# Optimization experiments

Hardware: AMD Instinct MI355X
Metric: run time of the kernel (lower is better)

## Reference

```python
import jax, jax.numpy as jnp
import numpy as np

N = 100000
E = 1600000
FEAT, COND, HID, LAT = 128, 32, 128, 64


def _init(key, shape, fan_in):
    # glorot-ish init, scale irrelevant for correctness baseline
    return jax.random.normal(key, shape, dtype=jnp.float32) / np.sqrt(fan_in)


def setup_inputs() -> dict:
    key = jax.random.key(0)
    ks = jax.random.split(key, 20)
    inp = {
        "feature": jax.random.normal(ks[0], (N, FEAT), dtype=jnp.float32),
        "condition": jax.random.normal(ks[1], (N, COND), dtype=jnp.float32),
        "noise": jax.random.normal(ks[2], (N, LAT), dtype=jnp.float32),
        "edge_index": jax.random.randint(ks[3], (2, E), 0, N, dtype=jnp.int64),
        # encoder GCNConv params (PyG convention: out = (norm-agg of x @ W) + b)
        "enc_i2h_W": _init(ks[4], (FEAT + COND, HID), FEAT + COND),
        "enc_i2h_b": jnp.zeros((HID,), jnp.float32),
        "enc_h2h_W": _init(ks[5], (HID, HID), HID),
        "enc_h2h_b": jnp.zeros((HID,), jnp.float32),
        "enc_mean_W": _init(ks[6], (HID, LAT), HID),
        "enc_mean_b": jnp.zeros((LAT,), jnp.float32),
        "enc_logvar_W": _init(ks[7], (HID, LAT), HID),
        "enc_logvar_b": jnp.zeros((LAT,), jnp.float32),
        # decoder GCNConv params
        "dec_i2h_W": _init(ks[8], (LAT + COND, HID), LAT + COND),
        "dec_i2h_b": jnp.zeros((HID,), jnp.float32),
        "dec_h2h_W": _init(ks[9], (HID, HID), HID),
        "dec_h2h_b": jnp.zeros((HID,), jnp.float32),
        "dec_out_W": _init(ks[10], (HID, FEAT), HID),
        "dec_out_b": jnp.zeros((FEAT,), jnp.float32),
    }
    return inp


def _gcn_prep(edge_index, n):
    # add self loops, compute symmetric normalization D^{-1/2} (A+I) D^{-1/2}
    loop = jnp.arange(n, dtype=edge_index.dtype)
    src = jnp.concatenate([edge_index[0], loop])  # [E+N]
    dst = jnp.concatenate([edge_index[1], loop])
    deg = jax.ops.segment_sum(jnp.ones_like(dst, dtype=jnp.float32), dst, num_segments=n)
    dis = jnp.where(deg > 0, jax.lax.rsqrt(deg), 0.0)
    norm = dis[src] * dis[dst]  # [E+N]
    return src, dst, norm


def _gcn_conv(x, W, b, src, dst, norm, n):
    h = x @ W                           # [N, out]
    msg = h[src] * norm[:, None]        # gather + scale, [E+N, out]
    out = jax.ops.segment_sum(msg, dst, num_segments=n)  # scatter-add
    return out + b


def reference(feature, condition, noise, edge_index,
              enc_i2h_W, enc_i2h_b, enc_h2h_W, enc_h2h_b,
              enc_mean_W, enc_mean_b, enc_logvar_W, enc_logvar_b,
              dec_i2h_W, dec_i2h_b, dec_h2h_W, dec_h2h_b,
              dec_out_W, dec_out_b):
    n = feature.shape[0]
    src, dst, norm = _gcn_prep(edge_index, n)
    # encoder
    x = jnp.concatenate([feature, condition], axis=1)
    h = jnp.tanh(_gcn_conv(x, enc_i2h_W, enc_i2h_b, src, dst, norm, n))
    h = jnp.tanh(_gcn_conv(h, enc_h2h_W, enc_h2h_b, src, dst, norm, n))
    mean = _gcn_conv(h, enc_mean_W, enc_mean_b, src, dst, norm, n)
    logvar = _gcn_conv(h, enc_logvar_W, enc_logvar_b, src, dst, norm, n)
    z = noise * jnp.exp(0.5 * logvar) + mean
    # decoder
    x2 = jnp.concatenate([z, condition], axis=1)
    g = jnp.tanh(_gcn_conv(x2, dec_i2h_W, dec_i2h_b, src, dst, norm, n))
    g = jnp.tanh(_gcn_conv(g, dec_h2h_W, dec_h2h_b, src, dst, norm, n))
    out = _gcn_conv(g, dec_out_W, dec_out_b, src, dst, norm, n)
    return (z, mean, logvar, out)
```

## Files before the change

### kernel.cpp

```cpp
#include <hip/hip_runtime.h>
#include <hip/hip_fp16.h>
#include <math.h>


#define FEAT 128
#define COND 32
#define HID  128
#define LAT  64

#define NG    8
#define RANGE 12500
#define BPG   32

typedef _Float16 f16x8 __attribute__((ext_vector_type(8)));
typedef float f32x4 __attribute__((ext_vector_type(4)));
typedef float floatx2 __attribute__((ext_vector_type(2)));

__device__ __forceinline__ uint pk2(float x, float y) {
  __half2 h = __floats2half2_rn(x, y);
  return __builtin_bit_cast(uint, h);
}
__device__ __forceinline__ floatx2 up8(uint u) {
  return __builtin_amdgcn_cvt_pk_f32_fp8(u, false);
}
__device__ __forceinline__ uint pk8(float a, float b) {
  return (uint)__builtin_amdgcn_cvt_pk_fp8_f32(a, b, 0, false);
}
__device__ __forceinline__ unsigned char pk8b(float a) {
  return (unsigned char)(pk8(a, a) & 0xff);
}

__global__ __launch_bounds__(256) void k_hist(const int* __restrict__ dstArr,
                                              int* __restrict__ part, int E, int n) {
  __shared__ int bins[RANGE];
  const int g = blockIdx.x & (NG - 1), bi = blockIdx.x >> 3;
  const int lo = g * RANGE;
  const int hi = min(n, lo + RANGE);
  for (int ii = threadIdx.x; ii < RANGE; ii += 256) bins[ii] = 0;
  __syncthreads();
  const int quads = E >> 2;
  const int per = (quads + BPG - 1) / BPG;
  const int q0 = bi * per, q1 = min(quads, q0 + per);
  const int4* d4 = (const int4*)dstArr;
  for (int q = q0 + threadIdx.x; q < q1; q += 256) {
    int4 d = d4[q];
    if (d.x >= lo && d.x < hi) atomicAdd(&bins[d.x - lo], 1);
    if (d.y >= lo && d.y < hi) atomicAdd(&bins[d.y - lo], 1);
    if (d.z >= lo && d.z < hi) atomicAdd(&bins[d.z - lo], 1);
    if (d.w >= lo && d.w < hi) atomicAdd(&bins[d.w - lo], 1);
  }
  if (bi == 0) {
    for (int e = (quads << 2) + threadIdx.x; e < E; e += 256) {
      int d = dstArr[e];
      if (d >= lo && d < hi) atomicAdd(&bins[d - lo], 1);
    }
  }
  __syncthreads();
  int* dst = part + (size_t)(g * BPG + bi) * RANGE;
  for (int ii = threadIdx.x; ii < RANGE; ii += 256) dst[ii] = bins[ii];
}

__global__ void k_scan1(const int* __restrict__ part, int* __restrict__ degI,
                        float* __restrict__ dis, int* __restrict__ ptr,
                        int* __restrict__ blkSum, int n) {
  __shared__ int wtot[4];
  int tid = threadIdx.x, lane = tid & 63, wid = tid >> 6;
  int base = blockIdx.x * 1024 + tid * 4;
  int v[4];
#pragma unroll
  for (int j = 0; j < 4; j++) {
    int i = base + j;
    int c = 0;
    if (i < n) {
      int g = i / RANGE, ii = i - g * RANGE;
      const int* p = part + (size_t)g * BPG * RANGE + ii;
      for (int b = 0; b < BPG; b++) c += p[(size_t)b * RANGE];
      degI[i] = c;
      dis[i] = rsqrtf((float)(c + 1));
    }
    v[j] = c;
  }
  int tsum = v[0] + v[1] + v[2] + v[3];
  int x = tsum;
#pragma unroll
  for (int off = 1; off < 64; off <<= 1) {
    int y = __shfl_up(x, off);
    if (lane >= off) x += y;
  }
  if (lane == 63) wtot[wid] = x;
  __syncthreads();
  int wbase = 0;
  for (int w = 0; w < wid; w++) wbase += wtot[w];
  int run = wbase + (x - tsum);
#pragma unroll
  for (int j = 0; j < 4; j++) {
    int i = base + j;
    if (i < n) ptr[i] = run;
    run += v[j];
  }
  if (tid == blockDim.x - 1) blkSum[blockIdx.x] = wbase + x;
}

__global__ void k_scan2(const int* __restrict__ blkSum, int* __restrict__ blkOff, int nb) {
  __shared__ int wtot[4];
  int tid = threadIdx.x, lane = tid & 63, wid = tid >> 6;
  int v = (tid < nb) ? blkSum[tid] : 0;
  int x = v;
#pragma unroll
  for (int off = 1; off < 64; off <<= 1) {
    int y = __shfl_up(x, off);
    if (lane >= off) x += y;
  }
  if (lane == 63) wtot[wid] = x;
  __syncthreads();
  int wbase = 0;
  for (int w = 0; w < wid; w++) wbase += wtot[w];
  if (tid < nb) blkOff[tid] = wbase + x - v;
}

__global__ void k_scan3(int* __restrict__ ptr, const int* __restrict__ blkOff, int n) {
  int i = blockIdx.x * blockDim.x + threadIdx.x;
  if (i < n) ptr[i] += blkOff[i >> 10];
}

__global__ void k_cum(int* __restrict__ part, const int* __restrict__ ptr, int n) {
  int i = blockIdx.x * blockDim.x + threadIdx.x;
  if (i >= n) return;
  int g = i / RANGE, ii = i - g * RANGE;
  int* p = part + (size_t)g * BPG * RANGE + ii;
  int run = ptr[i];
  for (int b = 0; b < BPG; b++) {
    int t = p[(size_t)b * RANGE];
    p[(size_t)b * RANGE] = run;
    run += t;
  }
}

__global__ __launch_bounds__(256) void k_fill2(const int* __restrict__ ei,
                                               const int* __restrict__ part,
                                               int* __restrict__ csr, int E, int n) {
  __shared__ int cur[RANGE];
  const int g = blockIdx.x & (NG - 1), bi = blockIdx.x >> 3;
  const int lo = g * RANGE;
  const int hi = min(n, lo + RANGE);
  const int* base = part + (size_t)(g * BPG + bi) * RANGE;
  for (int ii = threadIdx.x; ii < RANGE; ii += 256) cur[ii] = base[ii];
  __syncthreads();
  const int quads = E >> 2;
  const int per = (quads + BPG - 1) / BPG;
  const int q0 = bi * per, q1 = min(quads, q0 + per);
  const int4* s4 = (const int4*)ei;
  const int4* d4 = (const int4*)(ei + E);
  for (int q = q0 + threadIdx.x; q < q1; q += 256) {
    int4 s = s4[q], d = d4[q];
    if (d.x >= lo && d.x < hi) csr[atomicAdd(&cur[d.x - lo], 1)] = s.x;
    if (d.y >= lo && d.y < hi) csr[atomicAdd(&cur[d.y - lo], 1)] = s.y;
    if (d.z >= lo && d.z < hi) csr[atomicAdd(&cur[d.z - lo], 1)] = s.z;
    if (d.w >= lo && d.w < hi) csr[atomicAdd(&cur[d.w - lo], 1)] = s.w;
  }
  if (bi == 0) {
    for (int e = (quads << 2) + threadIdx.x; e < E; e += 256) {
      int d = ei[E + e];
      if (d >= lo && d < hi) csr[atomicAdd(&cur[d - lo], 1)] = ei[e];
    }
  }
}

__global__ void k_cast8(const float* __restrict__ src, uint* __restrict__ dst,
                        const float* __restrict__ dis, int n4) {
  int t = blockIdx.x * blockDim.x + threadIdx.x;
  if (t >= n4) return;
  size_t i4 = (size_t)t * 4;
  int row = (int)(i4 >> 5);
  float d = dis[row];
  float4 v = *(const float4*)&src[i4];
  uint r = (uint)__builtin_amdgcn_cvt_pk_fp8_f32(d * v.x, d * v.y, 0, false);
  r = (uint)__builtin_amdgcn_cvt_pk_fp8_f32(d * v.z, d * v.w, (int)r, true);
  dst[t] = r;
}

struct PW { const float* src; unsigned short* dst; int K, Ncols, colOff, NnTot; };
struct PWArr { PW d[7]; };

__global__ void k_packw(PWArr a) {
  PW d = a.d[blockIdx.y];
  int t = blockIdx.x * blockDim.x + threadIdx.x;
  if (t >= d.K * d.Ncols) return;
  int k = t / d.Ncols;
  int n = t - k * d.Ncols;
  float v = d.src[t];
  d.dst[((size_t)(k >> 3) * d.NnTot + d.colOff + n) * 8 + (k & 7)] =
      __builtin_bit_cast(unsigned short, (_Float16)v);
}

template <int W, int OUTK>
__global__ __launch_bounds__(256) void k_agg8(
    const unsigned char* __restrict__ X8, void* __restrict__ Yv,
    const int* __restrict__ degI, const float* __restrict__ dis,
    const int* __restrict__ ptr, const int* __restrict__ csr,
    const float* __restrict__ bias, int n) {
  constexpr int LPR = W / 2;
  constexpr int NB = 64 / LPR;
  __shared__ int idxs[4][72];
  const int wvw = threadIdx.x >> 6;
  const int l = threadIdx.x & 63;
  const int sub = l / LPR;
  const int boff = (l % LPR) * 2;
  const unsigned char* __restrict__ Xb = X8 + boff;
  const int stride = gridDim.x * 4;

  for (int i = blockIdx.x * 4 + wvw; i < n; i += stride) {
    const int p0 = ptr[i];
    const int cnt = degI[i];
    if (l < cnt) idxs[wvw][l] = csr[p0 + l];
    floatx2 acc;
    {
      uint u = *(const unsigned short*)(Xb + (size_t)i * W);
      floatx2 f = up8(u);
      acc.x = (sub == 0) ? f.x : 0.f;
      acc.y = (sub == 0) ? f.y : 0.f;
    }
    const int m = min(cnt, 64);
    int e = 0;
    if (NB == 1) {
      for (; e + 8 <= m; e += 8) {
        int4 q0 = *(const int4*)&idxs[wvw][e];
        int4 q1 = *(const int4*)&idxs[wvw][e + 4];
        uint u0 = *(const unsigned short*)(Xb + ((uint)q0.x << 7));
        uint u1 = *(const unsigned short*)(Xb + ((uint)q0.y << 7));
        uint u2 = *(const unsigned short*)(Xb + ((uint)q0.z << 7));
        uint u3 = *(const unsigned short*)(Xb + ((uint)q0.w << 7));
        uint u4 = *(const unsigned short*)(Xb + ((uint)q1.x << 7));
        uint u5 = *(const unsigned short*)(Xb + ((uint)q1.y << 7));
        uint u6 = *(const unsigned short*)(Xb + ((uint)q1.z << 7));
        uint u7 = *(const unsigned short*)(Xb + ((uint)q1.w << 7));
        acc += up8(u0) + up8(u1);
        acc += up8(u2) + up8(u3);
        acc += up8(u4) + up8(u5);
        acc += up8(u6) + up8(u7);
      }
      for (; e < m; ++e) {
        int s = idxs[wvw][e];
        acc += up8(*(const unsigned short*)(Xb + ((uint)s << 7)));
      }
      for (; e < cnt; ++e) {
        int s = csr[p0 + e];
        acc += up8(*(const unsigned short*)(Xb + ((uint)s << 7)));
      }
    } else {
      constexpr int SH = (W == 64) ? 6 : 5;
      for (; e + 4 * NB <= m; e += 4 * NB) {
        int s0 = idxs[wvw][e + sub];
        int s1 = idxs[wvw][e + NB + sub];
        int s2 = idxs[wvw][e + 2 * NB + sub];
        int s3 = idxs[wvw][e + 3 * NB + sub];
        uint u0 = *(const unsigned short*)(Xb + ((uint)s0 << SH));
        uint u1 = *(const unsigned short*)(Xb + ((uint)s1 << SH));
        uint u2 = *(const unsigned short*)(Xb + ((uint)s2 << SH));
        uint u3 = *(const unsigned short*)(Xb + ((uint)s3 << SH));
        acc += up8(u0) + up8(u1);
        acc += up8(u2) + up8(u3);
      }
      for (; e < m; e += NB) {
        int ii = e + sub;
        if (ii < m)
          acc += up8(*(const unsigned short*)(Xb + ((uint)idxs[wvw][ii] << SH)));
      }
      for (; e < cnt; e += NB) {
        int ii = e + sub;
        if (ii < cnt)
          acc += up8(*(const unsigned short*)(Xb + ((uint)csr[p0 + ii] << SH)));
      }
#pragma unroll
      for (int mask = LPR; mask < 64; mask <<= 1) {
        acc.x += __shfl_xor(acc.x, mask);
        acc.y += __shfl_xor(acc.y, mask);
      }
    }
    if (sub == 0) {
      float di = dis[i];
      float a0 = di * acc.x, a1 = di * acc.y;
      if (OUTK == 1) {
        float2 b = *(const float2*)&bias[boff];
        uint p = pk8(di * tanhf(a0 + b.x), di * tanhf(a1 + b.y));
        *(unsigned short*)((unsigned char*)Yv + (size_t)i * W + boff) =
            (unsigned short)p;
      } else {
        *(uint*)((unsigned char*)Yv + ((size_t)i * W + boff) * 2) = pk2(a0, a1);
      }
    }
  }
}

template <int KT, int MODE>
__global__ __launch_bounds__(256) void k_gemm16(
    const _Float16* __restrict__ A1, int K1,
    const _Float16* __restrict__ A2, int K2,
    const unsigned short* __restrict__ Wp,
    const float* __restrict__ b1, const float* __restrict__ b2,
    float* __restrict__ O1, float* __restrict__ O2, float* __restrict__ O3,
    unsigned char* __restrict__ O8,
    const float* __restrict__ noise, const float* __restrict__ dis, int M) {
  __shared__ unsigned short wl[(KT / 8) * 1024];
  const int tid = threadIdx.x;
  const int l = tid & 63, wid = tid >> 6;
  const int row0 = blockIdx.x * 128;
  constexpr int totalU16 = (KT / 8) * 1024;
  for (int o = tid * 8; o < totalU16; o += 256 * 8) {
    *(uint4*)&wl[o] = *(const uint4*)&Wp[o];
  }
  __syncthreads();

  const int ar = l & 15, kg = l >> 4;
  f32x4 acc[2][8] = {};
  for (int k0 = 0; k0 < KT; k0 += 32) {
    const _Float16* Ab;
    int kl, Kb;
    if (k0 < K1) { Ab = A1; kl = k0; Kb = K1; }
    else         { Ab = A2; kl = k0 - K1; Kb = K2; }
    f16x8 a[2];
#pragma unroll
    for (int mt = 0; mt < 2; mt++) {
      int row = row0 + wid * 32 + mt * 16 + ar;
      if (row < M) {
        a[mt] = *(const f16x8*)&Ab[(size_t)row * Kb + kl + kg * 8];
      } else {
#pragma unroll
        for (int j = 0; j < 8; j++) a[mt][j] = (_Float16)0;
      }
    }
    int lb = ((k0 >> 3) + kg) * 1024 + ar * 8;
#pragma unroll
    for (int nt = 0; nt < 8; nt++) {
      f16x8 b = *(const f16x8*)&wl[lb + nt * 128];
#pragma unroll
      for (int mt = 0; mt < 2; mt++)
        acc[mt][nt] = __builtin_amdgcn_mfma_f32_16x16x32_f16(a[mt], b, acc[mt][nt], 0, 0, 0);
    }
  }

#pragma unroll
  for (int mt = 0; mt < 2; mt++) {
    int rbase = row0 + wid * 32 + mt * 16 + (l >> 4) * 4;
#pragma unroll
    for (int r = 0; r < 4; r++) {
      int rw = rbase + r;
      if (rw >= M) continue;
      if (MODE == 1) {
        float dr = dis[rw];
#pragma unroll
        for (int nt = 0; nt < 4; nt++) {
          int c = nt * 16 + (l & 15);
          float mv = acc[mt][nt][r] + b1[c];
          float lv = acc[mt][nt + 4][r] + b2[c];
          O1[(size_t)rw * 64 + c] = mv;
          O2[(size_t)rw * 64 + c] = lv;
          float z = noise[(size_t)rw * 64 + c] * expf(0.5f * lv) + mv;
          O3[(size_t)rw * 64 + c] = z;
          O8[(size_t)rw * 64 + c] = pk8b(dr * z);
        }
      } else if (MODE == 0) {
        float dr = dis[rw];
#pragma unroll
        for (int nt = 0; nt < 8; nt++) {
          int c = nt * 16 + (l & 15);
          float v = tanhf(acc[mt][nt][r] + b1[c]);
          O8[(size_t)rw * 128 + c] = pk8b(dr * v);
        }
      } else {
#pragma unroll
        for (int nt = 0; nt < 8; nt++) {
          int c = nt * 16 + (l & 15);
          O1[(size_t)rw * 128 + c] = acc[mt][nt][r] + b1[c];
        }
      }
    }
  }
}

__global__ __launch_bounds__(256) void k_gemmP1(
    const float* __restrict__ F, const float* __restrict__ Cnd,
    const unsigned short* __restrict__ Wp, unsigned char* __restrict__ O8,
    const float* __restrict__ dis, int M) {
  __shared__ unsigned short wl[20 * 1024];
  const int tid = threadIdx.x;
  const int l = tid & 63, wid = tid >> 6;
  const int row0 = blockIdx.x * 128;
  for (int o = tid * 8; o < 20 * 1024; o += 256 * 8) {
    *(uint4*)&wl[o] = *(const uint4*)&Wp[o];
  }
  __syncthreads();

  const int ar = l & 15, kg = l >> 4;
  f32x4 acc[2][8] = {};
  for (int k0 = 0; k0 < 160; k0 += 32) {
    int col0 = k0 + kg * 8;
    f16x8 a[2];
#pragma unroll
    for (int mt = 0; mt < 2; mt++) {
      int row = row0 + wid * 32 + mt * 16 + ar;
      float4 u = {0, 0, 0, 0}, v = {0, 0, 0, 0};
      if (row < M) {
        if (col0 < 128) {
          u = *(const float4*)&F[(size_t)row * 128 + col0];
          v = *(const float4*)&F[(size_t)row * 128 + col0 + 4];
        } else {
          u = *(const float4*)&Cnd[(size_t)row * 32 + (col0 - 128)];
          v = *(const float4*)&Cnd[(size_t)row * 32 + (col0 - 124)];
        }
      }
      a[mt][0] = (_Float16)u.x; a[mt][1] = (_Float16)u.y;
      a[mt][2] = (_Float16)u.z; a[mt][3] = (_Float16)u.w;
      a[mt][4] = (_Float16)v.x; a[mt][5] = (_Float16)v.y;
      a[mt][6] = (_Float16)v.z; a[mt][7] = (_Float16)v.w;
    }
    int lb = ((k0 >> 3) + kg) * 1024 + ar * 8;
#pragma unroll
    for (int nt = 0; nt < 8; nt++) {
      f16x8 b = *(const f16x8*)&wl[lb + nt * 128];
#pragma unroll
      for (int mt = 0; mt < 2; mt++)
        acc[mt][nt] = __builtin_amdgcn_mfma_f32_16x16x32_f16(a[mt], b, acc[mt][nt], 0, 0, 0);
    }
  }
#pragma unroll
  for (int mt = 0; mt < 2; mt++) {
    int rbase = row0 + wid * 32 + mt * 16 + (l >> 4) * 4;
#pragma unroll
    for (int r = 0; r < 4; r++) {
      int rw = rbase + r;
      if (rw >= M) continue;
      float dr = dis[rw];
#pragma unroll
      for (int nt = 0; nt < 8; nt++) {
        int c = nt * 16 + (l & 15);
        O8[(size_t)rw * 128 + c] = pk8b(dr * acc[mt][nt][r]);
      }
    }
  }
}


static inline size_t align_up(size_t x, size_t a) { return (x + a - 1) & ~(a - 1); }

extern "C" void kernel_launch(void* const* d_in, const int* in_sizes, int n_in,
                              void* d_out, int out_size, void* d_ws, size_t ws_size,
                              hipStream_t stream) {
  const float* feature   = (const float*)d_in[0];
  const float* condition = (const float*)d_in[1];
  const float* noise     = (const float*)d_in[2];
  const int*   ei        = (const int*)d_in[3];
  const float* Wenc1 = (const float*)d_in[4];  const float* benc1 = (const float*)d_in[5];
  const float* Wenc2 = (const float*)d_in[6];  const float* benc2 = (const float*)d_in[7];
  const float* Wm    = (const float*)d_in[8];  const float* bm    = (const float*)d_in[9];
  const float* Wlv   = (const float*)d_in[10]; const float* blv   = (const float*)d_in[11];
  const float* Wd1   = (const float*)d_in[12]; const float* bd1   = (const float*)d_in[13];
  const float* Wd2   = (const float*)d_in[14]; const float* bd2   = (const float*)d_in[15];
  const float* Wout  = (const float*)d_in[16]; const float* bout  = (const float*)d_in[17];

  const int N = in_sizes[0] / FEAT;
  const int E = in_sizes[3] / 2;

  float* out = (float*)d_out;
  float* zseg    = out;
  float* meanseg = out + (size_t)N * LAT;
  float* lvseg   = out + (size_t)2 * N * LAT;
  float* outseg  = out + (size_t)3 * N * LAT;

  char* w = (char*)d_ws;
  size_t off = 0;
  int*   degI   = (int*)(w + off);   off = align_up(off + (size_t)N * 4, 256);
  float* dis    = (float*)(w + off); off = align_up(off + (size_t)N * 4, 256);
  int*   ptr    = (int*)(w + off);   off = align_up(off + (size_t)N * 4, 256);
  int*   blkSum = (int*)(w + off);   off = align_up(off + 4096, 256);
  int*   blkOff = (int*)(w + off);   off = align_up(off + 4096, 256);
  int*   csr    = (int*)(w + off);   off = align_up(off + (size_t)(E + 64) * 4, 256);
  unsigned short* WpE1 = (unsigned short*)(w + off); off = align_up(off + 160 * 128 * 2, 256);
  unsigned short* WpE2 = (unsigned short*)(w + off); off = align_up(off + 128 * 128 * 2, 256);
  unsigned short* WpML = (unsigned short*)(w + off); off = align_up(off + 128 * 128 * 2, 256);
  unsigned short* WpD1 = (unsigned short*)(w + off); off = align_up(off + 96 * 128 * 2, 256);
  unsigned short* WpD2 = (unsigned short*)(w + off); off = align_up(off + 128 * 128 * 2, 256);
  unsigned short* WpO  = (unsigned short*)(w + off); off = align_up(off + 128 * 128 * 2, 256);
  _Float16* S  = (_Float16*)(w + off); off = align_up(off + (size_t)N * 32 * 2, 256);
  _Float16* TA = (_Float16*)(w + off); off = align_up(off + (size_t)N * 128 * 2, 256);
  unsigned char* F8A = (unsigned char*)(w + off); off = align_up(off + (size_t)N * 128, 256);
  unsigned char* F8B = (unsigned char*)(w + off); off = align_up(off + (size_t)N * 128, 256);
  unsigned char* C8  = (unsigned char*)(w + off); off = align_up(off + (size_t)N * 32, 256);
  int* part = (int*)TA;

  const int TB_ = 256;
  dim3 blk(TB_);
  dim3 gN((N + TB_ - 1) / TB_);
  const int nScanBlk = (N + 1023) / 1024;
  dim3 gAgg(2048);
  dim3 gG((N + 127) / 128);
  dim3 gPart(NG * BPG);

  k_hist<<<gPart, blk, 0, stream>>>(ei + E, part, E, N);
  k_scan1<<<dim3(nScanBlk), blk, 0, stream>>>(part, degI, dis, ptr, blkSum, N);
  k_scan2<<<dim3(1), blk, 0, stream>>>(blkSum, blkOff, nScanBlk);
  k_scan3<<<gN, blk, 0, stream>>>(ptr, blkOff, N);
  k_cum<<<gN, blk, 0, stream>>>(part, ptr, N);
  k_fill2<<<gPart, blk, 0, stream>>>(ei, part, csr, E, N);

  k_cast8<<<dim3(((size_t)N * 32 / 4 + TB_ - 1) / TB_), blk, 0, stream>>>(
      condition, (uint*)C8, dis, N * 32 / 4);
  {
    PWArr pa;
    pa.d[0] = {Wenc1, WpE1, 160, 128, 0, 128};
    pa.d[1] = {Wenc2, WpE2, 128, 128, 0, 128};
    pa.d[2] = {Wm,    WpML, 128, 64,  0, 128};
    pa.d[3] = {Wlv,   WpML, 128, 64, 64, 128};
    pa.d[4] = {Wd1,   WpD1,  96, 128, 0, 128};
    pa.d[5] = {Wd2,   WpD2, 128, 128, 0, 128};
    pa.d[6] = {Wout,  WpO,  128, 128, 0, 128};
    k_packw<<<dim3(80, 7), blk, 0, stream>>>(pa);
  }

  k_gemmP1<<<gG, blk, 0, stream>>>(feature, condition, WpE1, F8A, dis, N);
  k_agg8<HID, 1><<<gAgg, blk, 0, stream>>>(F8A, F8B, degI, dis, ptr, csr, benc1, N);
  k_agg8<HID, 0><<<gAgg, blk, 0, stream>>>(F8B, TA, degI, dis, ptr, csr, nullptr, N);
  k_gemm16<128, 0><<<gG, blk, 0, stream>>>(
      TA, HID, nullptr, 0, WpE2, benc2, nullptr,
      nullptr, nullptr, nullptr, F8A, nullptr, dis, N);
  k_agg8<HID, 0><<<gAgg, blk, 0, stream>>>(F8A, TA, degI, dis, ptr, csr, nullptr, N);
  k_gemm16<128, 1><<<gG, blk, 0, stream>>>(
      TA, HID, nullptr, 0, WpML, bm, blv,
      meanseg, lvseg, zseg, F8B, noise, dis, N);

  k_agg8<LAT, 0><<<gAgg, blk, 0, stream>>>(F8B, TA, degI, dis, ptr, csr, nullptr, N);
  k_agg8<COND, 0><<<gAgg, blk, 0, stream>>>(C8, S, degI, dis, ptr, csr, nullptr, N);
  k_gemm16<96, 0><<<gG, blk, 0, stream>>>(
      TA, LAT, S, COND, WpD1, bd1, nullptr,
      nullptr, nullptr, nullptr, F8A, nullptr, dis, N);
  k_agg8<HID, 0><<<gAgg, blk, 0, stream>>>(F8A, TA, degI, dis, ptr, csr, nullptr, N);
  k_gemm16<128, 0><<<gG, blk, 0, stream>>>(
      TA, HID, nullptr, 0, WpD2, bd2, nullptr,
      nullptr, nullptr, nullptr, F8B, nullptr, dis, N);
  k_agg8<HID, 0><<<gAgg, blk, 0, stream>>>(F8B, TA, degI, dis, ptr, csr, nullptr, N);
  k_gemm16<128, 2><<<gG, blk, 0, stream>>>(
      TA, HID, nullptr, 0, WpO, bout, nullptr,
      outseg, nullptr, nullptr, nullptr, nullptr, dis, N);
}
```

Baseline: 614.1 us.

## Reorder decoder first layer to transform-then-aggregate via templated input GEMM

The decoder's first GCN layer used to aggregate z (64 wide) and condition (32 wide) separately, then run the 96-wide GEMM. Now it runs the GEMM on raw z and condition first, producing 128-wide fp8 features, and then aggregates with the fused bias+tanh aggregation used in the encoder. This drops the cast kernel, the condition aggregation and the z fp8 store. The catch is that the aggregation now runs at width 128 instead of 64+32, so there is more gather traffic.

Result: faster. 548.9 us (-10.6%).

```diff
diff --git a/kernel.cpp b/kernel.cpp
--- a/kernel.cpp
+++ b/kernel.cpp
@@ -164,19 +164,6 @@
       if (d >= lo && d < hi) csr[atomicAdd(&cur[d - lo], 1)] = ei[e];
     }
   }
-}
-
-__global__ void k_cast8(const float* __restrict__ src, uint* __restrict__ dst,
-                        const float* __restrict__ dis, int n4) {
-  int t = blockIdx.x * blockDim.x + threadIdx.x;
-  if (t >= n4) return;
-  size_t i4 = (size_t)t * 4;
-  int row = (int)(i4 >> 5);
-  float d = dis[row];
-  float4 v = *(const float4*)&src[i4];
-  uint r = (uint)__builtin_amdgcn_cvt_pk_fp8_f32(d * v.x, d * v.y, 0, false);
-  r = (uint)__builtin_amdgcn_cvt_pk_fp8_f32(d * v.z, d * v.w, (int)r, true);
-  dst[t] = r;
 }
 
 struct PW { const float* src; unsigned short* dst; int K, Ncols, colOff, NnTot; };
@@ -347,7 +334,6 @@
       int rw = rbase + r;
       if (rw >= M) continue;
       if (MODE == 1) {
-        float dr = dis[rw];
 #pragma unroll
         for (int nt = 0; nt < 4; nt++) {
           int c = nt * 16 + (l & 15);
@@ -357,7 +343,6 @@
           O2[(size_t)rw * 64 + c] = lv;
           float z = noise[(size_t)rw * 64 + c] * expf(0.5f * lv) + mv;
           O3[(size_t)rw * 64 + c] = z;
-          O8[(size_t)rw * 64 + c] = pk8b(dr * z);
         }
       } else if (MODE == 0) {
         float dr = dis[rw];
@@ -378,22 +363,25 @@
   }
 }
 
+template <int KT, int KA>
 __global__ __launch_bounds__(256) void k_gemmP1(
-    const float* __restrict__ F, const float* __restrict__ Cnd,
+    const float* __restrict__ A, const float* __restrict__ B,
     const unsigned short* __restrict__ Wp, unsigned char* __restrict__ O8,
     const float* __restrict__ dis, int M) {
-  __shared__ unsigned short wl[20 * 1024];
+  constexpr int KB = KT - KA;
+  __shared__ unsigned short wl[(KT / 8) * 1024];
   const int tid = threadIdx.x;
   const int l = tid & 63, wid = tid >> 6;
   const int row0 = blockIdx.x * 128;
-  for (int o = tid * 8; o < 20 * 1024; o += 256 * 8) {
+  constexpr int totalU16 = (KT / 8) * 1024;
+  for (int o = tid * 8; o < totalU16; o += 256 * 8) {
     *(uint4*)&wl[o] = *(const uint4*)&Wp[o];
   }
   __syncthreads();
 
   const int ar = l & 15, kg = l >> 4;
   f32x4 acc[2][8] = {};
-  for (int k0 = 0; k0 < 160; k0 += 32) {
+  for (int k0 = 0; k0 < KT; k0 += 32) {
     int col0 = k0 + kg * 8;
     f16x8 a[2];
 #pragma unroll
@@ -401,12 +389,12 @@
       int row = row0 + wid * 32 + mt * 16 + ar;
       float4 u = {0, 0, 0, 0}, v = {0, 0, 0, 0};
       if (row < M) {
-        if (col0 < 128) {
-          u = *(const float4*)&F[(size_t)row * 128 + col0];
-          v = *(const float4*)&F[(size_t)row * 128 + col0 + 4];
+        if (col0 < KA) {
+          u = *(const float4*)&A[(size_t)row * KA + col0];
+          v = *(const float4*)&A[(size_t)row * KA + col0 + 4];
         } else {
-          u = *(const float4*)&Cnd[(size_t)row * 32 + (col0 - 128)];
-          v = *(const float4*)&Cnd[(size_t)row * 32 + (col0 - 124)];
+          u = *(const float4*)&B[(size_t)row * KB + (col0 - KA)];
+          v = *(const float4*)&B[(size_t)row * KB + (col0 - KA + 4)];
         }
       }
       a[mt][0] = (_Float16)u.x; a[mt][1] = (_Float16)u.y;
@@ -481,11 +469,9 @@
   unsigned short* WpD1 = (unsigned short*)(w + off); off = align_up(off + 96 * 128 * 2, 256);
   unsigned short* WpD2 = (unsigned short*)(w + off); off = align_up(off + 128 * 128 * 2, 256);
   unsigned short* WpO  = (unsigned short*)(w + off); off = align_up(off + 128 * 128 * 2, 256);
-  _Float16* S  = (_Float16*)(w + off); off = align_up(off + (size_t)N * 32 * 2, 256);
   _Float16* TA = (_Float16*)(w + off); off = align_up(off + (size_t)N * 128 * 2, 256);
   unsigned char* F8A = (unsigned char*)(w + off); off = align_up(off + (size_t)N * 128, 256);
   unsigned char* F8B = (unsigned char*)(w + off); off = align_up(off + (size_t)N * 128, 256);
-  unsigned char* C8  = (unsigned char*)(w + off); off = align_up(off + (size_t)N * 32, 256);
   int* part = (int*)TA;
 
   const int TB_ = 256;
@@ -503,8 +489,6 @@
   k_cum<<<gN, blk, 0, stream>>>(part, ptr, N);
   k_fill2<<<gPart, blk, 0, stream>>>(ei, part, csr, E, N);
 
-  k_cast8<<<dim3(((size_t)N * 32 / 4 + TB_ - 1) / TB_), blk, 0, stream>>>(
-      condition, (uint*)C8, dis, N * 32 / 4);
   {
     PWArr pa;
     pa.d[0] = {Wenc1, WpE1, 160, 128, 0, 128};
@@ -517,7 +501,7 @@
     k_packw<<<dim3(80, 7), blk, 0, stream>>>(pa);
   }
 
-  k_gemmP1<<<gG, blk, 0, stream>>>(feature, condition, WpE1, F8A, dis, N);
+  k_gemmP1<160, 128><<<gG, blk, 0, stream>>>(feature, condition, WpE1, F8A, dis, N);
   k_agg8<HID, 1><<<gAgg, blk, 0, stream>>>(F8A, F8B, degI, dis, ptr, csr, benc1, N);
   k_agg8<HID, 0><<<gAgg, blk, 0, stream>>>(F8B, TA, degI, dis, ptr, csr, nullptr, N);
   k_gemm16<128, 0><<<gG, blk, 0, stream>>>(
@@ -526,18 +510,15 @@
   k_agg8<HID, 0><<<gAgg, blk, 0, stream>>>(F8A, TA, degI, dis, ptr, csr, nullptr, N);
   k_gemm16<128, 1><<<gG, blk, 0, stream>>>(
       TA, HID, nullptr, 0, WpML, bm, blv,
-      meanseg, lvseg, zseg, F8B, noise, dis, N);
-
-  k_agg8<LAT, 0><<<gAgg, blk, 0, stream>>>(F8B, TA, degI, dis, ptr, csr, nullptr, N);
-  k_agg8<COND, 0><<<gAgg, blk, 0, stream>>>(C8, S, degI, dis, ptr, csr, nullptr, N);
-  k_gemm16<96, 0><<<gG, blk, 0, stream>>>(
-      TA, LAT, S, COND, WpD1, bd1, nullptr,
+      meanseg, lvseg, zseg, nullptr, noise, dis, N);
+
+  k_gemmP1<96, 64><<<gG, blk, 0, stream>>>(zseg, condition, WpD1, F8A, dis, N);
+  k_agg8<HID, 1><<<gAgg, blk, 0, stream>>>(F8A, F8B, degI, dis, ptr, csr, bd1, N);
+  k_agg8<HID, 0><<<gAgg, blk, 0, stream>>>(F8B, TA, degI, dis, ptr, csr, nullptr, N);
+  k_gemm16<128, 0><<<gG, blk, 0, stream>>>(
+      TA, HID, nullptr, 0, WpD2, bd2, nullptr,
       nullptr, nullptr, nullptr, F8A, nullptr, dis, N);
   k_agg8<HID, 0><<<gAgg, blk, 0, stream>>>(F8A, TA, degI, dis, ptr, csr, nullptr, N);
-  k_gemm16<128, 0><<<gG, blk, 0, stream>>>(
-      TA, HID, nullptr, 0, WpD2, bd2, nullptr,
-      nullptr, nullptr, nullptr, F8B, nullptr, dis, N);
-  k_agg8<HID, 0><<<gAgg, blk, 0, stream>>>(F8B, TA, degI, dis, ptr, csr, nullptr, N);
   k_gemm16<128, 2><<<gG, blk, 0, stream>>>(
       TA, HID, nullptr, 0, WpO, bout, nullptr,
       outseg, nullptr, nullptr, nullptr, nullptr, dis, N);
```
